# Kernel tuning notes

Hardware: AMD Instinct MI355X
Metric: run time of the kernel (lower is better)

## Reference

```python
import jax, jax.numpy as jnp
import numpy as np

N_NODES = 50000
N_POOLED = 25000
N_EDGES = 800000
D = 64
NUM_LAYERS = 4
LN_EPS = 1e-5
LEAKY_SLOPE = 0.01


def setup_inputs() -> dict:
    key = jax.random.key(0)
    k_x, k_e, k_i, k_w = jax.random.split(key, 4)
    x = jax.random.normal(k_x, (N_POOLED, D), dtype=jnp.float32)
    edge_index = jax.random.randint(k_e, (2, N_EDGES), 0, N_NODES, dtype=jnp.int64)
    # unique sorted indices of kept nodes (as produced by top-k pooling)
    perm = jax.random.permutation(k_i, N_NODES)
    idx = jnp.sort(perm[:N_POOLED]).astype(jnp.int64)
    Ws = jax.random.normal(k_w, (NUM_LAYERS, D, D), dtype=jnp.float32) / np.sqrt(D)
    bs = jnp.zeros((NUM_LAYERS, D), dtype=jnp.float32)
    gammas = jnp.ones((NUM_LAYERS, D), dtype=jnp.float32)
    betas = jnp.zeros((NUM_LAYERS, D), dtype=jnp.float32)
    return {"x": x, "edge_index": edge_index, "idx": idx,
            "Ws": Ws, "bs": bs, "gammas": gammas, "betas": betas}


def _layer_norm(x, gamma, beta):
    mu = jnp.mean(x, axis=-1, keepdims=True)
    xc = x - mu
    var = jnp.mean(xc * xc, axis=-1, keepdims=True)
    return xc * jax.lax.rsqrt(var + LN_EPS) * gamma + beta


def reference(x, edge_index, idx, Ws, bs, gammas, betas):
    # Unpool (layer 0): scatter pooled features into full-size zero tensor.
    cur = jnp.zeros((N_NODES, D), dtype=x.dtype).at[idx].set(x)

    # GCN normalization with self loops (shared across layers; graph is fixed).
    loop = jnp.arange(N_NODES, dtype=edge_index.dtype)
    src = jnp.concatenate([edge_index[0], loop])
    dst = jnp.concatenate([edge_index[1], loop])
    deg = jax.ops.segment_sum(jnp.ones_like(dst, dtype=x.dtype), dst,
                              num_segments=N_NODES)
    dinv = jax.lax.rsqrt(jnp.maximum(deg, 1.0))  # deg >= 1 (self loops)
    norm = (dinv[src] * dinv[dst])[:, None]      # [E+N, 1]

    h = None
    for l in range(NUM_LAYERS):
        # GCNConv: X W, then D^{-1/2}(A+I)D^{-1/2} aggregation, then bias.
        xw = cur @ Ws[l]
        agg = jax.ops.segment_sum(xw[src] * norm, dst, num_segments=N_NODES)
        agg = agg + bs[l]
        y = _layer_norm(agg, gammas[l], betas[l])
        act = jnp.where(y > 0, y, LEAKY_SLOPE * y)  # LeakyReLU(0.01)
        # dropout p=0.3 is identity in eval mode
        h = act * 0.5 if h is None else h + act * 0.5
        cur = act  # subsequent unpools are identity (sizes already match)
    return h
```

## Files before the change

### kernel.cpp

```cpp
#include <hip/hip_runtime.h>
#include <hip/hip_fp16.h>

#define NN 50000
#define NP 25000
#define NE 800000
#define DD 64
#define NL 4
#define CSR_CAP (NE + 7 * NN + 16)


__device__ __forceinline__ ushort f2bf(float f) {
    unsigned u = __float_as_uint(f);
    unsigned r = (u + 0x7fffu + ((u >> 16) & 1u)) >> 16;
    return (ushort)r;
}

__device__ __forceinline__ float4 bf4_to_f4(uint a, uint b) {
    float4 r;
    r.x = __uint_as_float(a << 16);
    r.y = __uint_as_float(a & 0xffff0000u);
    r.z = __uint_as_float(b << 16);
    r.w = __uint_as_float(b & 0xffff0000u);
    return r;
}

__device__ __forceinline__ float4 ld_bf16x4(const uint2* p) {
    uint2 q = *p;
    return bf4_to_f4(q.x, q.y);
}


__global__ void count_edges_k(const int* __restrict__ dst, int* __restrict__ cnt,
                              int* __restrict__ rank, int E) {
    int e = blockIdx.x * 256 + threadIdx.x;
    if (e < E) rank[e] = atomicAdd(&cnt[dst[e]], 1);
}

__global__ void scan_local_k(const int* __restrict__ cnt, int* __restrict__ rowptr,
                             int* __restrict__ bsum, int n) {
    __shared__ int tmp[1024];
    int t = threadIdx.x;
    int i = blockIdx.x * 1024 + t;
    int v = (i < n) ? ((cnt[i] + 7) & ~7) : 0;
    tmp[t] = v;
    __syncthreads();
    for (int off = 1; off < 1024; off <<= 1) {
        int a = (t >= off) ? tmp[t - off] : 0;
        __syncthreads();
        tmp[t] += a;
        __syncthreads();
    }
    if (i < n) rowptr[i] = tmp[t] - v;
    if (t == 1023) bsum[blockIdx.x] = tmp[1023];
}

__global__ void scan_sums_k(int* bsum, int nb, int* rowptr, int n) {
    int t = threadIdx.x;
    int v = (t < nb) ? bsum[t] : 0;
    int s = v;
#pragma unroll
    for (int o = 1; o < 64; o <<= 1) {
        int u = __shfl_up(s, o);
        if (t >= o) s += u;
    }
    if (t < nb) bsum[t] = s - v;
    if (t == nb - 1) rowptr[n] = s;
}

__global__ void finalize_k(int* __restrict__ rowptr, const int* __restrict__ bsum,
                           const int* __restrict__ cnt, float* __restrict__ dinv, int n) {
    int i = blockIdx.x * 1024 + threadIdx.x;
    if (i < n) {
        rowptr[i] += bsum[blockIdx.x];
        dinv[i] = rsqrtf((float)(cnt[i] + 1));
    }
}

__global__ void fill_scatter_k(const int* __restrict__ src, const int* __restrict__ dst,
                               const int* __restrict__ rank, const int* __restrict__ rowptr,
                               const float* __restrict__ dinv, uint* __restrict__ csr,
                               const float4* __restrict__ x4, const int* __restrict__ idx,
                               ushort4* __restrict__ c0) {
    int b = blockIdx.x;
    if (b < 3125) {
        int e = b * 256 + threadIdx.x;
        int s = src[e], d = dst[e];
        int p = rowptr[d] + rank[e];
        float w = dinv[s] * dinv[d];
        uint h = (uint)__half_as_ushort(__float2half_rn(w));
        csr[p] = (uint)s | (h << 16);
    } else {
        int i = (b - 3125) * 256 + threadIdx.x;
        if (i >= NP * 16) return;
        int row = i >> 4, q = i & 15;
        float4 v = x4[i];
        ushort4 o;
        o.x = f2bf(v.x); o.y = f2bf(v.y); o.z = f2bf(v.z); o.w = f2bf(v.w);
        c0[(size_t)idx[row] * 16 + q] = o;
    }
}


__global__ void gemm64_k(const uint2* __restrict__ in2, const float* __restrict__ W,
                         ushort* __restrict__ out) {
    __shared__ float sW[64][64];
    __shared__ float srow[16][64];
    int t = threadIdx.x;
    const float4* W4 = (const float4*)W;
    float4* sW4 = (float4*)sW;
#pragma unroll
    for (int j = 0; j < 4; ++j) sW4[t + 256 * j] = W4[t + 256 * j];
    int r0 = blockIdx.x * 16;
    float4 val = ld_bf16x4(in2 + (size_t)r0 * 16 + t);
    *(float4*)&srow[t >> 4][4 * (t & 15)] = val;
    __syncthreads();
    int r = t >> 4;
    int c4 = (t & 15) * 4;
    float ax = 0.f, ay = 0.f, az = 0.f, aw = 0.f;
#pragma unroll
    for (int k = 0; k < 64; ++k) {
        float a = srow[r][k];
        float4 w = *(const float4*)&sW[k][c4];
        ax += a * w.x; ay += a * w.y; az += a * w.z; aw += a * w.w;
    }
    ushort4 o;
    o.x = f2bf(ax); o.y = f2bf(ay); o.z = f2bf(az); o.w = f2bf(aw);
    *(ushort4*)&out[(size_t)(r0 + r) * 64 + c4] = o;
}


__global__ void agg_ln_k(const uint4* __restrict__ xw4, const int* __restrict__ rowptr,
                         const uint* __restrict__ csr, const float* __restrict__ dinv,
                         const float4* __restrict__ bias4, const float4* __restrict__ gamma4,
                         const float4* __restrict__ beta4, uint4* next,
                         const uint4* c1, const uint4* c2, const uint4* c3,
                         float4* outp, int last) {
    int tid = threadIdx.x;
    int l8 = tid & 7;
    int v = blockIdx.x * 32 + (tid >> 3);
    if (v >= NN) return;
    const uint4* csrq = (const uint4*)csr;
    float dv = dinv[v];
    int jb = rowptr[v], je = rowptr[v + 1];
    float4 aLo, aHi;
    {
        uint4 q = xw4[(size_t)v * 8 + l8];
        float4 lo = bf4_to_f4(q.x, q.y), hi = bf4_to_f4(q.z, q.w);
        float s = dv * dv;
        aLo.x = s * lo.x; aLo.y = s * lo.y; aLo.z = s * lo.z; aLo.w = s * lo.w;
        aHi.x = s * hi.x; aHi.y = s * hi.y; aHi.z = s * hi.z; aHi.w = s * hi.w;
    }
    uint4 ca = csrq[jb >> 2];
    uint4 cb = csrq[(jb >> 2) + 1];
#define WGT(E)  __half2float(__ushort_as_half((ushort)((E) >> 16)))
    for (int j = jb; j < je; j += 8) {
        uint4 na = csrq[(j >> 2) + 2];
        uint4 nb = csrq[(j >> 2) + 3];
        uint4 q0 = xw4[(size_t)(ca.x & 0xffffu) * 8 + l8];
        uint4 q1 = xw4[(size_t)(ca.y & 0xffffu) * 8 + l8];
        uint4 q2 = xw4[(size_t)(ca.z & 0xffffu) * 8 + l8];
        uint4 q3 = xw4[(size_t)(ca.w & 0xffffu) * 8 + l8];
        uint4 q4 = xw4[(size_t)(cb.x & 0xffffu) * 8 + l8];
        uint4 q5 = xw4[(size_t)(cb.y & 0xffffu) * 8 + l8];
        uint4 q6 = xw4[(size_t)(cb.z & 0xffffu) * 8 + l8];
        uint4 q7 = xw4[(size_t)(cb.w & 0xffffu) * 8 + l8];
        float w0 = WGT(ca.x), w1 = WGT(ca.y), w2 = WGT(ca.z), w3 = WGT(ca.w);
        float w4 = WGT(cb.x), w5 = WGT(cb.y), w6 = WGT(cb.z), w7 = WGT(cb.w);
#define ACC(Q, W) { \
        float4 lo = bf4_to_f4(Q.x, Q.y), hi = bf4_to_f4(Q.z, Q.w); \
        aLo.x += W * lo.x; aLo.y += W * lo.y; aLo.z += W * lo.z; aLo.w += W * lo.w; \
        aHi.x += W * hi.x; aHi.y += W * hi.y; aHi.z += W * hi.z; aHi.w += W * hi.w; }
        ACC(q0, w0) ACC(q1, w1) ACC(q2, w2) ACC(q3, w3)
        ACC(q4, w4) ACC(q5, w5) ACC(q6, w6) ACC(q7, w7)
#undef ACC
        ca = na; cb = nb;
    }
#undef WGT
    float4 bLo = bias4[2 * l8], bBhi = bias4[2 * l8 + 1];
    aLo.x += bLo.x; aLo.y += bLo.y; aLo.z += bLo.z; aLo.w += bLo.w;
    aHi.x += bBhi.x; aHi.y += bBhi.y; aHi.z += bBhi.z; aHi.w += bBhi.w;
    float s = aLo.x + aLo.y + aLo.z + aLo.w + aHi.x + aHi.y + aHi.z + aHi.w;
#pragma unroll
    for (int o = 1; o <= 4; o <<= 1) s += __shfl_xor(s, o);
    float mu = s * (1.0f / 64.0f);
    float4 cLo = make_float4(aLo.x - mu, aLo.y - mu, aLo.z - mu, aLo.w - mu);
    float4 cHi = make_float4(aHi.x - mu, aHi.y - mu, aHi.z - mu, aHi.w - mu);
    float q2v = cLo.x * cLo.x + cLo.y * cLo.y + cLo.z * cLo.z + cLo.w * cLo.w
              + cHi.x * cHi.x + cHi.y * cHi.y + cHi.z * cHi.z + cHi.w * cHi.w;
#pragma unroll
    for (int o = 1; o <= 4; o <<= 1) q2v += __shfl_xor(q2v, o);
    float rs = rsqrtf(q2v * (1.0f / 64.0f) + 1e-5f);
    float4 gLo = gamma4[2 * l8], gHi = gamma4[2 * l8 + 1];
    float4 tLo = beta4[2 * l8],  tHi = beta4[2 * l8 + 1];
    float4 yLo = make_float4(cLo.x * rs * gLo.x + tLo.x, cLo.y * rs * gLo.y + tLo.y,
                             cLo.z * rs * gLo.z + tLo.z, cLo.w * rs * gLo.w + tLo.w);
    float4 yHi = make_float4(cHi.x * rs * gHi.x + tHi.x, cHi.y * rs * gHi.y + tHi.y,
                             cHi.z * rs * gHi.z + tHi.z, cHi.w * rs * gHi.w + tHi.w);
    float4 eLo = make_float4(yLo.x > 0.f ? yLo.x : 0.01f * yLo.x,
                             yLo.y > 0.f ? yLo.y : 0.01f * yLo.y,
                             yLo.z > 0.f ? yLo.z : 0.01f * yLo.z,
                             yLo.w > 0.f ? yLo.w : 0.01f * yLo.w);
    float4 eHi = make_float4(yHi.x > 0.f ? yHi.x : 0.01f * yHi.x,
                             yHi.y > 0.f ? yHi.y : 0.01f * yHi.y,
                             yHi.z > 0.f ? yHi.z : 0.01f * yHi.z,
                             yHi.w > 0.f ? yHi.w : 0.01f * yHi.w);
    if (!last) {
        uint4 o;
        o.x = (uint)f2bf(eLo.x) | ((uint)f2bf(eLo.y) << 16);
        o.y = (uint)f2bf(eLo.z) | ((uint)f2bf(eLo.w) << 16);
        o.z = (uint)f2bf(eHi.x) | ((uint)f2bf(eHi.y) << 16);
        o.w = (uint)f2bf(eHi.z) | ((uint)f2bf(eHi.w) << 16);
        next[(size_t)v * 8 + l8] = o;
    } else {
        uint4 u1 = c1[(size_t)v * 8 + l8];
        uint4 u2 = c2[(size_t)v * 8 + l8];
        uint4 u3 = c3[(size_t)v * 8 + l8];
        float4 p1 = bf4_to_f4(u1.x, u1.y), p1h = bf4_to_f4(u1.z, u1.w);
        float4 p2 = bf4_to_f4(u2.x, u2.y), p2h = bf4_to_f4(u2.z, u2.w);
        float4 p3 = bf4_to_f4(u3.x, u3.y), p3h = bf4_to_f4(u3.z, u3.w);
        float4 oLo, oHi;
        oLo.x = 0.5f * (p1.x + p2.x + p3.x + eLo.x);
        oLo.y = 0.5f * (p1.y + p2.y + p3.y + eLo.y);
        oLo.z = 0.5f * (p1.z + p2.z + p3.z + eLo.z);
        oLo.w = 0.5f * (p1.w + p2.w + p3.w + eLo.w);
        oHi.x = 0.5f * (p1h.x + p2h.x + p3h.x + eHi.x);
        oHi.y = 0.5f * (p1h.y + p2h.y + p3h.y + eHi.y);
        oHi.z = 0.5f * (p1h.z + p2h.z + p3h.z + eHi.z);
        oHi.w = 0.5f * (p1h.w + p2h.w + p3h.w + eHi.w);
        outp[(size_t)v * 16 + 2 * l8]     = oLo;
        outp[(size_t)v * 16 + 2 * l8 + 1] = oHi;
    }
}


extern "C" void kernel_launch(void* const* d_in, const int* in_sizes, int n_in,
                              void* d_out, int out_size, void* d_ws, size_t ws_size,
                              hipStream_t stream) {
    const float* x      = (const float*)d_in[0];
    const int*   ei     = (const int*)d_in[1];
    const int*   src    = ei;
    const int*   dst    = ei + NE;
    const int*   idx    = (const int*)d_in[2];
    const float* Ws     = (const float*)d_in[3];
    const float* bs     = (const float*)d_in[4];
    const float* gammas = (const float*)d_in[5];
    const float* betas  = (const float*)d_in[6];
    float* out = (float*)d_out;

    char* w = (char*)d_ws;
    auto alloc = [&](size_t bytes) -> char* {
        char* p = w;
        w += (bytes + 255) & ~(size_t)255;
        return p;
    };
    ushort* c[NL];
    for (int l = 0; l < NL; ++l) c[l] = (ushort*)alloc((size_t)NN * 64 * 2);
    ushort* xw    = (ushort*)alloc((size_t)NN * 64 * 2);
    int*   cnt    = (int*)alloc((size_t)NN * 4);
    int*   rowptr = (int*)alloc((size_t)(NN + 1) * 4);
    int*   rank   = (int*)alloc((size_t)NE * 4);
    float* dinv   = (float*)alloc((size_t)NN * 4);
    int*   bsum   = (int*)alloc(64 * 4);
    uint*  csr    = (uint*)alloc((size_t)CSR_CAP * 4);

    hipMemsetAsync(cnt, 0, (size_t)NN * 4, stream);
    hipMemsetAsync(c[0], 0, (size_t)NN * 64 * 2, stream);
    hipMemsetAsync(csr, 0, (size_t)CSR_CAP * 4, stream);

    count_edges_k<<<(NE + 255) / 256, 256, 0, stream>>>(dst, cnt, rank, NE);
    int nb = (NN + 1023) / 1024;
    scan_local_k<<<nb, 1024, 0, stream>>>(cnt, rowptr, bsum, NN);
    scan_sums_k<<<1, 64, 0, stream>>>(bsum, nb, rowptr, NN);
    finalize_k<<<nb, 1024, 0, stream>>>(rowptr, bsum, cnt, dinv, NN);
    fill_scatter_k<<<3125 + 1563, 256, 0, stream>>>(src, dst, rank, rowptr, dinv, csr,
                                                    (const float4*)x, idx, (ushort4*)c[0]);

    int agrid = (NN + 31) / 32;
    for (int l = 0; l < NL; ++l) {
        gemm64_k<<<NN / 16, 256, 0, stream>>>((const uint2*)c[l], Ws + (size_t)l * 64 * 64,
                                              xw);
        int last = (l == NL - 1);
        agg_ln_k<<<agrid, 256, 0, stream>>>((const uint4*)xw, rowptr, csr, dinv,
                                            (const float4*)(bs + l * 64),
                                            (const float4*)(gammas + l * 64),
                                            (const float4*)(betas + l * 64),
                                            last ? nullptr : (uint4*)c[l + 1],
                                            (const uint4*)c[1], (const uint4*)c[2],
                                            (const uint4*)c[3], (float4*)out, last);
    }
}
```

Baseline: 209.0 us.

## Bucket nodes by degree and process aggregation in degree-sorted order

Builds a histogram of per-node in-degree buckets (in units of 8 edges) during the scan, computes bucket offsets, and writes a permutation that groups nodes of similar degree. The aggregation kernel then maps each 8-lane group to a node via this permutation. This is meant to reduce wavefront divergence from uneven loop trip counts across neighbouring nodes. The cost is an extra kernel, one extra indirection per node, and loss of the natural locality of output writes and row pointer reads.

Result: slower. 214.0 us (+2.4%).

```diff
diff --git a/kernel.cpp b/kernel.cpp
--- a/kernel.cpp
+++ b/kernel.cpp
@@ -37,13 +37,17 @@
 }
 
 __global__ void scan_local_k(const int* __restrict__ cnt, int* __restrict__ rowptr,
-                             int* __restrict__ bsum, int n) {
+                             int* __restrict__ bsum, int* __restrict__ ghist, int n) {
     __shared__ int tmp[1024];
+    __shared__ int lh[8];
     int t = threadIdx.x;
     int i = blockIdx.x * 1024 + t;
-    int v = (i < n) ? ((cnt[i] + 7) & ~7) : 0;
+    int c = (i < n) ? cnt[i] : 0;
+    int v = (i < n) ? ((c + 7) & ~7) : 0;
     tmp[t] = v;
-    __syncthreads();
+    if (t < 8) lh[t] = 0;
+    __syncthreads();
+    if (i < n) atomicAdd(&lh[min((c + 7) >> 3, 7)], 1);
     for (int off = 1; off < 1024; off <<= 1) {
         int a = (t >= off) ? tmp[t - off] : 0;
         __syncthreads();
@@ -52,9 +56,11 @@
     }
     if (i < n) rowptr[i] = tmp[t] - v;
     if (t == 1023) bsum[blockIdx.x] = tmp[1023];
-}
-
-__global__ void scan_sums_k(int* bsum, int nb, int* rowptr, int n) {
+    if (t < 8) atomicAdd(&ghist[t], lh[t]);
+}
+
+__global__ void scan_sums_k(int* bsum, int nb, int* rowptr, int n,
+                            const int* __restrict__ ghist, int* __restrict__ gcursor) {
     int t = threadIdx.x;
     int v = (t < nb) ? bsum[t] : 0;
     int s = v;
@@ -65,6 +71,10 @@
     }
     if (t < nb) bsum[t] = s - v;
     if (t == nb - 1) rowptr[n] = s;
+    if (t == 0) {
+        int run = 0;
+        for (int b = 0; b < 8; ++b) { int h = ghist[b]; gcursor[b] = run; run += h; }
+    }
 }
 
 __global__ void finalize_k(int* __restrict__ rowptr, const int* __restrict__ bsum,
@@ -74,6 +84,26 @@
         rowptr[i] += bsum[blockIdx.x];
         dinv[i] = rsqrtf((float)(cnt[i] + 1));
     }
+}
+
+__global__ void perm_k(const int* __restrict__ cnt, int* __restrict__ gcursor,
+                       int* __restrict__ perm, int n) {
+    __shared__ int lcnt[8];
+    __shared__ int lbase[8];
+    int t = threadIdx.x;
+    int i = blockIdx.x * 1024 + t;
+    if (t < 8) lcnt[t] = 0;
+    __syncthreads();
+    int bin = 0, r = 0;
+    bool valid = (i < n);
+    if (valid) {
+        bin = min((cnt[i] + 7) >> 3, 7);
+        r = atomicAdd(&lcnt[bin], 1);
+    }
+    __syncthreads();
+    if (t < 8) lbase[t] = atomicAdd(&gcursor[t], lcnt[t]);
+    __syncthreads();
+    if (valid) perm[lbase[bin] + r] = i;
 }
 
 __global__ void fill_scatter_k(const int* __restrict__ src, const int* __restrict__ dst,
@@ -131,14 +161,16 @@
 
 __global__ void agg_ln_k(const uint4* __restrict__ xw4, const int* __restrict__ rowptr,
                          const uint* __restrict__ csr, const float* __restrict__ dinv,
+                         const int* __restrict__ perm,
                          const float4* __restrict__ bias4, const float4* __restrict__ gamma4,
                          const float4* __restrict__ beta4, uint4* next,
                          const uint4* c1, const uint4* c2, const uint4* c3,
                          float4* outp, int last) {
     int tid = threadIdx.x;
     int l8 = tid & 7;
-    int v = blockIdx.x * 32 + (tid >> 3);
-    if (v >= NN) return;
+    int slot = blockIdx.x * 32 + (tid >> 3);
+    if (slot >= NN) return;
+    int v = perm[slot];
     const uint4* csrq = (const uint4*)csr;
     float dv = dinv[v];
     int jb = rowptr[v], je = rowptr[v + 1];
@@ -255,23 +287,28 @@
     };
     ushort* c[NL];
     for (int l = 0; l < NL; ++l) c[l] = (ushort*)alloc((size_t)NN * 64 * 2);
-    ushort* xw    = (ushort*)alloc((size_t)NN * 64 * 2);
-    int*   cnt    = (int*)alloc((size_t)NN * 4);
-    int*   rowptr = (int*)alloc((size_t)(NN + 1) * 4);
-    int*   rank   = (int*)alloc((size_t)NE * 4);
-    float* dinv   = (float*)alloc((size_t)NN * 4);
-    int*   bsum   = (int*)alloc(64 * 4);
-    uint*  csr    = (uint*)alloc((size_t)CSR_CAP * 4);
+    ushort* xw     = (ushort*)alloc((size_t)NN * 64 * 2);
+    int*    cnt    = (int*)alloc((size_t)NN * 4);
+    int*    rowptr = (int*)alloc((size_t)(NN + 1) * 4);
+    int*    rank   = (int*)alloc((size_t)NE * 4);
+    float*  dinv   = (float*)alloc((size_t)NN * 4);
+    int*    bsum   = (int*)alloc(64 * 4);
+    int*    ghist  = (int*)alloc(8 * 4);
+    int*    gcursor= (int*)alloc(8 * 4);
+    int*    perm   = (int*)alloc((size_t)NN * 4);
+    uint*   csr    = (uint*)alloc((size_t)CSR_CAP * 4);
 
     hipMemsetAsync(cnt, 0, (size_t)NN * 4, stream);
     hipMemsetAsync(c[0], 0, (size_t)NN * 64 * 2, stream);
     hipMemsetAsync(csr, 0, (size_t)CSR_CAP * 4, stream);
+    hipMemsetAsync(ghist, 0, 8 * 4, stream);
 
     count_edges_k<<<(NE + 255) / 256, 256, 0, stream>>>(dst, cnt, rank, NE);
     int nb = (NN + 1023) / 1024;
-    scan_local_k<<<nb, 1024, 0, stream>>>(cnt, rowptr, bsum, NN);
-    scan_sums_k<<<1, 64, 0, stream>>>(bsum, nb, rowptr, NN);
+    scan_local_k<<<nb, 1024, 0, stream>>>(cnt, rowptr, bsum, ghist, NN);
+    scan_sums_k<<<1, 64, 0, stream>>>(bsum, nb, rowptr, NN, ghist, gcursor);
     finalize_k<<<nb, 1024, 0, stream>>>(rowptr, bsum, cnt, dinv, NN);
+    perm_k<<<nb, 1024, 0, stream>>>(cnt, gcursor, perm, NN);
     fill_scatter_k<<<3125 + 1563, 256, 0, stream>>>(src, dst, rank, rowptr, dinv, csr,
                                                     (const float4*)x, idx, (ushort4*)c[0]);
 
@@ -280,7 +317,7 @@
         gemm64_k<<<NN / 16, 256, 0, stream>>>((const uint2*)c[l], Ws + (size_t)l * 64 * 64,
                                               xw);
         int last = (l == NL - 1);
-        agg_ln_k<<<agrid, 256, 0, stream>>>((const uint4*)xw, rowptr, csr, dinv,
+        agg_ln_k<<<agrid, 256, 0, stream>>>((const uint4*)xw, rowptr, csr, dinv, perm,
                                             (const float4*)(bs + l * 64),
                                             (const float4*)(gammas + l * 64),
                                             (const float4*)(betas + l * 64),
```

## Split each node's aggregation across two thread octets and drop finalize kernel

Applied to the files above, without the earlier changes.

The aggregation kernel now assigns 16 threads per node, with two octets processing alternating 8-edge chunks and combining partials via a lane shuffle. This aims to expose more memory-level parallelism for the gathers, at the cost of losing the CSR prefetch and leaving half the threads idle during the epilogue. The scan finalize kernel is removed by adding block sums where rowptr is consumed. The three memsets are merged into one contiguous memset, and the gemm shared row buffer is padded.

New measurement: 340.0 us. +62.6%, slower.

```diff
diff --git a/kernel.cpp b/kernel.cpp
--- a/kernel.cpp
+++ b/kernel.cpp
@@ -6,7 +6,7 @@
 #define NE 800000
 #define DD 64
 #define NL 4
-#define CSR_CAP (NE + 7 * NN + 16)
+#define CSR_CAP (NE + 7 * NN + 64)
 
 
 __device__ __forceinline__ ushort f2bf(float f) {
@@ -37,11 +37,12 @@
 }
 
 __global__ void scan_local_k(const int* __restrict__ cnt, int* __restrict__ rowptr,
-                             int* __restrict__ bsum, int n) {
+                             int* __restrict__ bsum, float* __restrict__ dinv, int n) {
     __shared__ int tmp[1024];
     int t = threadIdx.x;
     int i = blockIdx.x * 1024 + t;
-    int v = (i < n) ? ((cnt[i] + 7) & ~7) : 0;
+    int c = (i < n) ? cnt[i] : 0;
+    int v = (i < n) ? ((c + 7) & ~7) : 0;
     tmp[t] = v;
     __syncthreads();
     for (int off = 1; off < 1024; off <<= 1) {
@@ -50,11 +51,15 @@
         tmp[t] += a;
         __syncthreads();
     }
-    if (i < n) rowptr[i] = tmp[t] - v;
+    if (i < n) {
+        rowptr[i] = tmp[t] - v;
+        dinv[i] = rsqrtf((float)(c + 1));
+        if (i == n - 1) rowptr[n] = tmp[t];
+    }
     if (t == 1023) bsum[blockIdx.x] = tmp[1023];
 }
 
-__global__ void scan_sums_k(int* bsum, int nb, int* rowptr, int n) {
+__global__ void scan_sums_k(int* bsum, int nb) {
     int t = threadIdx.x;
     int v = (t < nb) ? bsum[t] : 0;
     int s = v;
@@ -64,20 +69,11 @@
         if (t >= o) s += u;
     }
     if (t < nb) bsum[t] = s - v;
-    if (t == nb - 1) rowptr[n] = s;
-}
-
-__global__ void finalize_k(int* __restrict__ rowptr, const int* __restrict__ bsum,
-                           const int* __restrict__ cnt, float* __restrict__ dinv, int n) {
-    int i = blockIdx.x * 1024 + threadIdx.x;
-    if (i < n) {
-        rowptr[i] += bsum[blockIdx.x];
-        dinv[i] = rsqrtf((float)(cnt[i] + 1));
-    }
 }
 
 __global__ void fill_scatter_k(const int* __restrict__ src, const int* __restrict__ dst,
                                const int* __restrict__ rank, const int* __restrict__ rowptr,
+                               const int* __restrict__ bsum,
                                const float* __restrict__ dinv, uint* __restrict__ csr,
                                const float4* __restrict__ x4, const int* __restrict__ idx,
                                ushort4* __restrict__ c0) {
@@ -85,7 +81,7 @@
     if (b < 3125) {
         int e = b * 256 + threadIdx.x;
         int s = src[e], d = dst[e];
-        int p = rowptr[d] + rank[e];
+        int p = rowptr[d] + bsum[d >> 10] + rank[e];
         float w = dinv[s] * dinv[d];
         uint h = (uint)__half_as_ushort(__float2half_rn(w));
         csr[p] = (uint)s | (h << 16);
@@ -104,7 +100,7 @@
 __global__ void gemm64_k(const uint2* __restrict__ in2, const float* __restrict__ W,
                          ushort* __restrict__ out) {
     __shared__ float sW[64][64];
-    __shared__ float srow[16][64];
+    __shared__ float srow[16][65];
     int t = threadIdx.x;
     const float4* W4 = (const float4*)W;
     float4* sW4 = (float4*)sW;
@@ -129,33 +125,36 @@
 }
 
 
-__global__ void agg_ln_k(const uint4* __restrict__ xw4, const int* __restrict__ rowptr,
-                         const uint* __restrict__ csr, const float* __restrict__ dinv,
-                         const float4* __restrict__ bias4, const float4* __restrict__ gamma4,
-                         const float4* __restrict__ beta4, uint4* next,
-                         const uint4* c1, const uint4* c2, const uint4* c3,
-                         float4* outp, int last) {
+__global__ void __launch_bounds__(256, 8)
+agg_ln_k(const uint4* __restrict__ xw4, const int* __restrict__ rowptr,
+         const int* __restrict__ bsum,
+         const uint* __restrict__ csr, const float* __restrict__ dinv,
+         const float4* __restrict__ bias4, const float4* __restrict__ gamma4,
+         const float4* __restrict__ beta4, uint4* next,
+         const uint4* c1, const uint4* c2, const uint4* c3,
+         float4* outp, int last) {
     int tid = threadIdx.x;
     int l8 = tid & 7;
-    int v = blockIdx.x * 32 + (tid >> 3);
+    int oct = (tid >> 3) & 1;
+    int v = blockIdx.x * 16 + (tid >> 4);
     if (v >= NN) return;
     const uint4* csrq = (const uint4*)csr;
-    float dv = dinv[v];
-    int jb = rowptr[v], je = rowptr[v + 1];
-    float4 aLo, aHi;
-    {
+    int jb = rowptr[v] + bsum[v >> 10];
+    int je = rowptr[v + 1] + bsum[(v + 1) >> 10];
+    float4 aLo = make_float4(0.f, 0.f, 0.f, 0.f);
+    float4 aHi = make_float4(0.f, 0.f, 0.f, 0.f);
+    if (!oct) {
+        float dv = dinv[v];
         uint4 q = xw4[(size_t)v * 8 + l8];
         float4 lo = bf4_to_f4(q.x, q.y), hi = bf4_to_f4(q.z, q.w);
         float s = dv * dv;
         aLo.x = s * lo.x; aLo.y = s * lo.y; aLo.z = s * lo.z; aLo.w = s * lo.w;
         aHi.x = s * hi.x; aHi.y = s * hi.y; aHi.z = s * hi.z; aHi.w = s * hi.w;
     }
-    uint4 ca = csrq[jb >> 2];
-    uint4 cb = csrq[(jb >> 2) + 1];
 #define WGT(E)  __half2float(__ushort_as_half((ushort)((E) >> 16)))
-    for (int j = jb; j < je; j += 8) {
-        uint4 na = csrq[(j >> 2) + 2];
-        uint4 nb = csrq[(j >> 2) + 3];
+    for (int j = jb + oct * 8; j < je; j += 16) {
+        const uint4* cp = csrq + (j >> 2);
+        uint4 ca = cp[0], cb = cp[1];
         uint4 q0 = xw4[(size_t)(ca.x & 0xffffu) * 8 + l8];
         uint4 q1 = xw4[(size_t)(ca.y & 0xffffu) * 8 + l8];
         uint4 q2 = xw4[(size_t)(ca.z & 0xffffu) * 8 + l8];
@@ -173,9 +172,12 @@
         ACC(q0, w0) ACC(q1, w1) ACC(q2, w2) ACC(q3, w3)
         ACC(q4, w4) ACC(q5, w5) ACC(q6, w6) ACC(q7, w7)
 #undef ACC
-        ca = na; cb = nb;
     }
 #undef WGT
+    aLo.x += __shfl_xor(aLo.x, 8); aLo.y += __shfl_xor(aLo.y, 8);
+    aLo.z += __shfl_xor(aLo.z, 8); aLo.w += __shfl_xor(aLo.w, 8);
+    aHi.x += __shfl_xor(aHi.x, 8); aHi.y += __shfl_xor(aHi.y, 8);
+    aHi.z += __shfl_xor(aHi.z, 8); aHi.w += __shfl_xor(aHi.w, 8);
     float4 bLo = bias4[2 * l8], bBhi = bias4[2 * l8 + 1];
     aLo.x += bLo.x; aLo.y += bLo.y; aLo.z += bLo.z; aLo.w += bLo.w;
     aHi.x += bBhi.x; aHi.y += bBhi.y; aHi.z += bBhi.z; aHi.w += bBhi.w;
@@ -190,6 +192,7 @@
 #pragma unroll
     for (int o = 1; o <= 4; o <<= 1) q2v += __shfl_xor(q2v, o);
     float rs = rsqrtf(q2v * (1.0f / 64.0f) + 1e-5f);
+    if (oct) return;
     float4 gLo = gamma4[2 * l8], gHi = gamma4[2 * l8 + 1];
     float4 tLo = beta4[2 * l8],  tHi = beta4[2 * l8 + 1];
     float4 yLo = make_float4(cLo.x * rs * gLo.x + tLo.x, cLo.y * rs * gLo.y + tLo.y,
@@ -253,34 +256,36 @@
         w += (bytes + 255) & ~(size_t)255;
         return p;
     };
+    char*   zbase  = w;
+    int*    cnt    = (int*)alloc((size_t)NN * 4);
+    uint*   csr    = (uint*)alloc((size_t)CSR_CAP * 4);
+    ushort* c0     = (ushort*)alloc((size_t)NN * 64 * 2);
+    size_t  zbytes = (size_t)(w - zbase);
     ushort* c[NL];
-    for (int l = 0; l < NL; ++l) c[l] = (ushort*)alloc((size_t)NN * 64 * 2);
-    ushort* xw    = (ushort*)alloc((size_t)NN * 64 * 2);
-    int*   cnt    = (int*)alloc((size_t)NN * 4);
-    int*   rowptr = (int*)alloc((size_t)(NN + 1) * 4);
-    int*   rank   = (int*)alloc((size_t)NE * 4);
-    float* dinv   = (float*)alloc((size_t)NN * 4);
-    int*   bsum   = (int*)alloc(64 * 4);
-    uint*  csr    = (uint*)alloc((size_t)CSR_CAP * 4);
-
-    hipMemsetAsync(cnt, 0, (size_t)NN * 4, stream);
-    hipMemsetAsync(c[0], 0, (size_t)NN * 64 * 2, stream);
-    hipMemsetAsync(csr, 0, (size_t)CSR_CAP * 4, stream);
+    c[0] = c0;
+    for (int l = 1; l < NL; ++l) c[l] = (ushort*)alloc((size_t)NN * 64 * 2);
+    ushort* xw     = (ushort*)alloc((size_t)NN * 64 * 2);
+    int*    rowptr = (int*)alloc((size_t)(NN + 1) * 4);
+    int*    rank   = (int*)alloc((size_t)NE * 4);
+    float*  dinv   = (float*)alloc((size_t)NN * 4);
+    int*    bsum   = (int*)alloc(64 * 4);
+
+    hipMemsetAsync(zbase, 0, zbytes, stream);
 
     count_edges_k<<<(NE + 255) / 256, 256, 0, stream>>>(dst, cnt, rank, NE);
     int nb = (NN + 1023) / 1024;
-    scan_local_k<<<nb, 1024, 0, stream>>>(cnt, rowptr, bsum, NN);
-    scan_sums_k<<<1, 64, 0, stream>>>(bsum, nb, rowptr, NN);
-    finalize_k<<<nb, 1024, 0, stream>>>(rowptr, bsum, cnt, dinv, NN);
-    fill_scatter_k<<<3125 + 1563, 256, 0, stream>>>(src, dst, rank, rowptr, dinv, csr,
-                                                    (const float4*)x, idx, (ushort4*)c[0]);
-
-    int agrid = (NN + 31) / 32;
+    scan_local_k<<<nb, 1024, 0, stream>>>(cnt, rowptr, bsum, dinv, NN);
+    scan_sums_k<<<1, 64, 0, stream>>>(bsum, nb);
+    fill_scatter_k<<<3125 + 1563, 256, 0, stream>>>(src, dst, rank, rowptr, bsum, dinv,
+                                                    csr, (const float4*)x, idx,
+                                                    (ushort4*)c[0]);
+
+    int agrid = (NN + 15) / 16;
     for (int l = 0; l < NL; ++l) {
         gemm64_k<<<NN / 16, 256, 0, stream>>>((const uint2*)c[l], Ws + (size_t)l * 64 * 64,
                                               xw);
         int last = (l == NL - 1);
-        agg_ln_k<<<agrid, 256, 0, stream>>>((const uint4*)xw, rowptr, csr, dinv,
+        agg_ln_k<<<agrid, 256, 0, stream>>>((const uint4*)xw, rowptr, bsum, csr, dinv,
                                             (const float4*)(bs + l * 64),
                                             (const float4*)(gammas + l * 64),
                                             (const float4*)(betas + l * 64),
```
